# Kernel optimization log

Hardware: AMD Instinct MI355X
Metric: run time of the kernel (lower is better)

The kernel has to match this reference:

```python
import jax, jax.numpy as jnp
import numpy as np

E = 2  # expand_ratio


def _linear_scan(u, a):
    """h_t = a_t * h_{t-1} + u_t along axis 0, h_{-1}=0. Parallel associative scan."""
    def comb(x, y):
        a1, b1 = x
        a2, b2 = y
        return a2 * a1, a2 * b1 + b2
    _, h = jax.lax.associative_scan(comb, (a, u), axis=0)
    return h


def setup_inputs() -> dict:
    key = jax.random.key(0)
    ks = jax.random.split(key, 8)
    n, b, d = 2048, 4, 1024
    s = 1.0 / np.sqrt(d)
    return {
        "x": jax.random.normal(ks[0], (n, b, d), jnp.float32),
        "lower_bound": jax.random.uniform(ks[1], (d,), jnp.float32),
        "W_in": jax.random.normal(ks[2], (d, 3 * d), jnp.float32) * s,
        "b_in": jnp.zeros((3 * d,), jnp.float32),
        "W_out": jax.random.normal(ks[3], (d, d), jnp.float32) * s,
        "b_out": jnp.zeros((d,), jnp.float32),
        "gamma": jnp.ones((d,), jnp.float32),
        "beta": jnp.zeros((d,), jnp.float32),
    }


def reference(x, lower_bound, W_in, b_in, W_out, b_out, gamma, beta):
    n, b, d = x.shape
    h = d // E
    feat = x @ W_in + b_in                      # (n,b,3d)
    inp, og, fg = jnp.split(feat, 3, axis=-1)
    inp = jax.nn.silu(inp)
    og = jax.nn.sigmoid(og)
    fg = jax.nn.sigmoid(fg)
    # reshape (h d) -> h, d=E
    inp = inp.reshape(n, b, h, E)
    og = og.reshape(n, b, h, E)
    fg = fg.reshape(n, b, h, E)
    lb = lower_bound.reshape(h, E)
    lam = lb + (1.0 - lb) * fg                  # (n,b,h,E)
    # outer-product input: (1-lam) outer inp over the E dims -> (n,b,h,E,E)
    u = jnp.einsum('nbhd,nbhe->nbhde', 1.0 - lam, inp)
    a = jnp.broadcast_to(lam[..., None], u.shape)
    u = u.reshape(n, b, h * E * E)
    a = a.reshape(n, b, h * E * E)
    state_fwd = _linear_scan(u, a)
    state_rev = jnp.flip(_linear_scan(jnp.flip(u, 0), jnp.flip(a, 0)), 0)
    state = (state_fwd + state_rev).reshape(n, b, h, E, E)
    out = jnp.einsum('nbhde,nbhd->nbhe', state, og).reshape(n, b, d)
    # layernorm over last dim
    mu = jnp.mean(out, axis=-1, keepdims=True)
    var = jnp.var(out, axis=-1, keepdims=True)
    out = (out - mu) * jax.lax.rsqrt(var + 1e-5) * gamma + beta
    return out @ W_out + b_out
```

## Files before the change

### kernel.cpp

```cpp
#include <hip/hip_runtime.h>

typedef __bf16 bf16x8 __attribute__((ext_vector_type(8)));
typedef float floatx4 __attribute__((ext_vector_type(4)));

#define NCH 128
#define CLEN 16

__device__ __forceinline__ unsigned short f2bf(float f) {
  unsigned int u = __builtin_bit_cast(unsigned int, f);
  u += 0x7fff + ((u >> 16) & 1);
  return (unsigned short)(u >> 16);
}
__device__ __forceinline__ float bf2f(unsigned short u) {
  unsigned int v = (unsigned int)u << 16;
  return __builtin_bit_cast(float, v);
}
__device__ __forceinline__ float bf2f_lo(unsigned int u) {
  return __builtin_bit_cast(float, u << 16);
}
__device__ __forceinline__ float bf2f_hi(unsigned int u) {
  return __builtin_bit_cast(float, u & 0xffff0000u);
}

__device__ __forceinline__ void async_copy16(const void* g, void* l) {
  __builtin_amdgcn_global_load_lds(
      (const __attribute__((address_space(1))) unsigned int*)g,
      (__attribute__((address_space(3))) unsigned int*)l, 16, 0, 0);
}

__global__ void prep_kernel(const float* __restrict__ x, unsigned short* __restrict__ x_bf,
                            const float* __restrict__ Win, unsigned short* __restrict__ winT,
                            const float* __restrict__ Wout, unsigned short* __restrict__ woutT) {
  __shared__ float tile[32][33];
  const int bx = blockIdx.x;
  const int tid = threadIdx.x;
  if (bx < 8192) {
    int i = bx * 256 + tid;
    float4 v = ((const float4*)x)[i];
    ushort4 o;
    o.x = f2bf(v.x); o.y = f2bf(v.y); o.z = f2bf(v.z); o.w = f2bf(v.w);
    ((ushort4*)x_bf)[i] = o;
    return;
  }
  const float* W;
  unsigned short* WT;
  int ncols, n0, k0;
  if (bx < 8192 + 3072) {
    int t2 = bx - 8192;
    W = Win; WT = winT; ncols = 3072;
    n0 = (t2 % 96) * 32; k0 = (t2 / 96) * 32;
  } else {
    int t2 = bx - 8192 - 3072;
    W = Wout; WT = woutT; ncols = 1024;
    n0 = (t2 & 31) * 32; k0 = (t2 >> 5) * 32;
  }
  const int tx = tid & 31, tyb = tid >> 5;
#pragma unroll
  for (int r = 0; r < 4; r++) {
    int ty = tyb + r * 8;
    tile[ty][tx] = W[(size_t)(k0 + ty) * ncols + n0 + tx];
  }
  __syncthreads();
#pragma unroll
  for (int r = 0; r < 4; r++) {
    int ty = tyb + r * 8;
    WT[(size_t)(n0 + ty) * 1024 + k0 + tx] = f2bf(tile[tx][ty]);
  }
}

template <int EPI>
__global__ __launch_bounds__(512, 2) void gemm1_kernel(
    const unsigned short* __restrict__ A, const unsigned short* __restrict__ BT,
    const float* __restrict__ bias, const float* __restrict__ lb,
    float* __restrict__ outf,
    unsigned short* __restrict__ o_inp, unsigned short* __restrict__ o_og,
    unsigned short* __restrict__ o_om) {
  __shared__ alignas(16) char smem[147456];
  const int orig = blockIdx.x;
  const int wg = (EPI == 1) ? (orig & 7) * 96 + (orig >> 3)
                            : (orig & 7) * 32 + (orig >> 3);
  const int m0 = (wg & 63) << 7;
  const int n0 = (wg >> 6) << 8;
  const int tid = threadIdx.x;
  const int lane = tid & 63, wave = tid >> 6;
  const int wm = wave >> 2, wn = wave & 3;
  const int srow = tid >> 3;
  const int sq = (tid & 7) ^ (srow & 7);
  const unsigned short* gA = A + (size_t)(m0 + srow) * 1024 + sq * 8;
  const unsigned short* gB = BT + (size_t)(n0 + srow) * 1024 + sq * 8;
  char* lw = smem + wave * 1024;
  const int aro = (wm * 64 + (lane & 15)) * 128;
  const int bro = (wn * 64 + (lane & 15)) * 128;
  const int qs0 = ((lane >> 4) ^ (lane & 7)) * 16;
  const int qs1 = ((4 + (lane >> 4)) ^ (lane & 7)) * 16;

  floatx4 acc[4][4] = {};
  bf16x8 aF[4][2], bF[4][2];

#define STG(lofs, gh, kk)                                \
  do {                                                   \
    const unsigned short* _g = (gh) + (size_t)(kk) * 64; \
    async_copy16(_g, lw + (lofs));                       \
    async_copy16(_g + 65536, lw + (lofs) + 8192);        \
  } while (0)
#define RA(base, i, s) \
  (*(const bf16x8*)(smem + (base) + aro + (i) * 2048 + ((s) ? qs1 : qs0)))
#define RB(base, j, s) \
  (*(const bf16x8*)(smem + (base) + bro + (j) * 2048 + ((s) ? qs1 : qs0)))
#define BAR __builtin_amdgcn_s_barrier()
#define LGKM0 asm volatile("s_waitcnt lgkmcnt(0)" ::: "memory")
#define VM6 asm volatile("s_waitcnt vmcnt(6)" ::: "memory")
#define MM(d, a, b) d = __builtin_amdgcn_mfma_f32_16x16x32_bf16(a, b, d, 0, 0, 0)

#define TILE(AB, BB, SA, SB, kk)                                               \
  do {                                                                         \
    _Pragma("unroll") for (int i = 0; i < 4; i++) {                            \
      aF[i][0] = RA(AB, i, 0); aF[i][1] = RA(AB, i, 1);                        \
    }                                                                          \
    _Pragma("unroll") for (int j = 0; j < 2; j++) {                            \
      bF[j][0] = RB(BB, j, 0); bF[j][1] = RB(BB, j, 1);                        \
    }                                                                          \
    STG(SA, gA, kk);                                                           \
    STG(SB, gB, kk);                                                           \
    BAR; LGKM0;                                                                \
    __builtin_amdgcn_s_setprio(1);                                             \
    _Pragma("unroll") for (int i = 0; i < 4; i++) {                            \
      _Pragma("unroll") for (int j = 0; j < 2; j++) {                          \
        MM(acc[i][j], aF[i][0], bF[j][0]); MM(acc[i][j], aF[i][1], bF[j][1]);  \
      }                                                                        \
    }                                                                          \
    __builtin_amdgcn_s_setprio(0);                                             \
    BAR;                                                                       \
    _Pragma("unroll") for (int j = 2; j < 4; j++) {                            \
      bF[j][0] = RB(BB, j, 0); bF[j][1] = RB(BB, j, 1);                        \
    }                                                                          \
    STG((SB) + 16384, gB + 131072, kk);                                        \
    BAR; LGKM0;                                                                \
    __builtin_amdgcn_s_setprio(1);                                             \
    _Pragma("unroll") for (int i = 0; i < 4; i++) {                            \
      _Pragma("unroll") for (int j = 2; j < 4; j++) {                          \
        MM(acc[i][j], aF[i][0], bF[j][0]); MM(acc[i][j], aF[i][1], bF[j][1]);  \
      }                                                                        \
    }                                                                          \
    __builtin_amdgcn_s_setprio(0);                                             \
    VM6; BAR;                                                                  \
  } while (0)

  STG(0, gA, 0);
  STG(49152, gB, 0);
  STG(49152 + 16384, gB + 131072, 0);
  STG(16384, gA, 1);
  STG(81920, gB, 1);
  STG(81920 + 16384, gB + 131072, 1);
  VM6;
  BAR;

#pragma unroll 1
  for (int tt = 0; tt < 15; tt += 3) {
    TILE(0, 49152, 32768, 114688, tt + 2);
    TILE(16384, 81920, 0, 49152, tt + 3);
    TILE(32768, 114688, 16384, 81920, (tt + 4 > 15 ? 15 : tt + 4));
  }
  TILE(0, 49152, 32768, 114688, 15);
#undef STG
#undef RA
#undef RB
#undef BAR
#undef LGKM0
#undef VM6
#undef MM
#undef TILE

  asm volatile("s_waitcnt vmcnt(0) lgkmcnt(0)" ::: "memory");
  const int lrw = wm * 16 + (lane >> 4) * 4;
  const int lcw = wn * 64 + (lane & 15);
  const int er = tid >> 4, ec = (tid & 15) * 16;
  const int growb = m0 + (er >> 4) * 64 + (er & 15);
  float bi[4];
#pragma unroll
  for (int j = 0; j < 4; j++) bi[j] = bias[n0 + wn * 64 + j * 16 + (lane & 15)];
  if (EPI == 1) {
    const int seg = n0 >> 10;
    unsigned short* dst = (seg == 0) ? o_inp : (seg == 1) ? o_og : o_om;
    unsigned short* Cs = (unsigned short*)smem;
    float Lv[4];
#pragma unroll
    for (int j = 0; j < 4; j++)
      Lv[j] = (seg == 2) ? lb[(n0 + wn * 64 + j * 16 + (lane & 15)) & 1023] : 0.f;
#pragma unroll
    for (int i = 0; i < 4; i++) {
      __syncthreads();
#pragma unroll
      for (int j = 0; j < 4; j++)
#pragma unroll
        for (int g = 0; g < 4; g++) {
          float v = acc[i][j][g] + bi[j];
          unsigned short ob;
          if (seg == 0) { float s = 1.f / (1.f + __expf(-v)); ob = f2bf(v * s); }
          else if (seg == 1) { float s = 1.f / (1.f + __expf(-v)); ob = f2bf(s); }
          else { float sm = 1.f / (1.f + __expf(v)); ob = f2bf((1.f - Lv[j]) * sm); }
          Cs[(lrw + g) * 264 + lcw + j * 16] = ob;
        }
      __syncthreads();
      uint4 v0 = *(uint4*)&Cs[er * 264 + ec];
      uint4 v1 = *(uint4*)&Cs[er * 264 + ec + 8];
      size_t ro = (size_t)(growb + i * 16) * 1024 + (n0 & 1023) + ec;
      *(uint4*)&dst[ro] = v0;
      *(uint4*)&dst[ro + 8] = v1;
    }
  } else {
    float* Cf = (float*)smem;
#pragma unroll
    for (int i = 0; i < 4; i++) {
      __syncthreads();
#pragma unroll
      for (int j = 0; j < 4; j++)
#pragma unroll
        for (int g = 0; g < 4; g++)
          Cf[(lrw + g) * 264 + lcw + j * 16] = acc[i][j][g] + bi[j];
      __syncthreads();
      size_t ro = (size_t)(growb + i * 16) * 1024 + n0 + ec;
#pragma unroll
      for (int k = 0; k < 4; k++) {
        float4 v = *(float4*)&Cf[er * 264 + ec + k * 4];
        *(float4*)&outf[ro + k * 4] = v;
      }
    }
  }
}

__global__ void scan_passA(const unsigned short* __restrict__ om, const unsigned short* __restrict__ ip,
                           float* __restrict__ sumA, float* __restrict__ sumBf,
                           float* __restrict__ sumBr) {
  int idx = blockIdx.x * 256 + threadIdx.x;
  int h = idx & 511, cb = idx >> 9, b = cb & 3, c = cb >> 2;
  long base = ((long)c * CLEN * 4 + b) * 1024 + 2 * h;
  float p0 = 1.f, p1 = 1.f;
  float s00 = 0.f, s01 = 0.f, s10 = 0.f, s11 = 0.f;
  float r00 = 0.f, r01 = 0.f, r10 = 0.f, r11 = 0.f;
#pragma unroll
  for (int t = 0; t < CLEN; t++) {
    ushort2 l2 = *(const ushort2*)(om + base);
    ushort2 i2 = *(const ushort2*)(ip + base);
    base += 4096;
    float omx = bf2f(l2.x), omy = bf2f(l2.y);
    float ipx = bf2f(i2.x), ipy = bf2f(i2.y);
    float lx = 1.f - omx, ly = 1.f - omy;
    float u00 = omx * ipx, u01 = omx * ipy, u10 = omy * ipx, u11 = omy * ipy;
    r00 += p0 * u00; r01 += p0 * u01; r10 += p1 * u10; r11 += p1 * u11;
    s00 = lx * s00 + u00; s01 = lx * s01 + u01;
    s10 = ly * s10 + u10; s11 = ly * s11 + u11;
    p0 *= lx; p1 *= ly;
  }
  ((float2*)sumA)[idx] = make_float2(p0, p1);
  ((float4*)sumBf)[idx] = make_float4(s00, s01, s10, s11);
  ((float4*)sumBr)[idx] = make_float4(r00, r01, r10, r11);
}

__global__ void scan_b1(const float* __restrict__ sumA, const float* __restrict__ sumBf,
                        const float* __restrict__ sumBr,
                        float* __restrict__ superA, float* __restrict__ superB) {
  int t = blockIdx.x * 256 + threadIdx.x;
  int ch = t & 3, bh = (t >> 2) & 2047, sc = (t >> 13) & 7, dir = t >> 16;
  int dd = ch >> 1;
  float Acc = 1.f, Bcc = 0.f;
  if (dir == 0) {
    for (int i = 0; i < 16; i++) {
      int si = (sc * 16 + i) * 2048 + bh;
      float a = sumA[(size_t)si * 2 + dd];
      float b = sumBf[(size_t)si * 4 + ch];
      Bcc = a * Bcc + b;
      Acc *= a;
    }
  } else {
    for (int i = 15; i >= 0; i--) {
      int si = (sc * 16 + i) * 2048 + bh;
      float a = sumA[(size_t)si * 2 + dd];
      float b = sumBr[(size_t)si * 4 + ch];
      Bcc = a * Bcc + b;
      Acc *= a;
    }
  }
  superA[t] = Acc;
  superB[t] = Bcc;
}

__global__ void scan_b3(const float* __restrict__ sumA, const float* __restrict__ sumBf,
                        const float* __restrict__ sumBr,
                        const float* __restrict__ superA, const float* __restrict__ superB,
                        float* __restrict__ initF, float* __restrict__ initR) {
  int t = blockIdx.x * 256 + threadIdx.x;
  int ch = t & 3, bh = (t >> 2) & 2047, sc = (t >> 13) & 7, dir = t >> 16;
  int dd = ch >> 1;
  float H = 0.f;
  if (dir == 0) {
    for (int s = 0; s < sc; s++) {
      size_t idx = ((size_t)s * 2048 + bh) * 4 + ch;
      H = superA[idx] * H + superB[idx];
    }
    for (int i = 0; i < 16; i++) {
      int si = (sc * 16 + i) * 2048 + bh;
      initF[(size_t)si * 4 + ch] = H;
      H = sumA[(size_t)si * 2 + dd] * H + sumBf[(size_t)si * 4 + ch];
    }
  } else {
    for (int s = 7; s > sc; s--) {
      size_t idx = ((size_t)(8 + s) * 2048 + bh) * 4 + ch;
      H = superA[idx] * H + superB[idx];
    }
    for (int i = 15; i >= 0; i--) {
      int si = (sc * 16 + i) * 2048 + bh;
      initR[(size_t)si * 4 + ch] = H;
      H = sumA[(size_t)si * 2 + dd] * H + sumBr[(size_t)si * 4 + ch];
    }
  }
}

__global__ __launch_bounds__(512) void scanC_ln_kernel(
    const unsigned short* __restrict__ om, const unsigned short* __restrict__ ip,
    const unsigned short* __restrict__ og,
    const float* __restrict__ initF, const float* __restrict__ initR,
    const float* __restrict__ gamma, const float* __restrict__ beta,
    unsigned short* __restrict__ ybf) {
  __shared__ float tile[8][1024];
  __shared__ float ldsG[1024];
  __shared__ float ldsB[1024];
  const int h = threadIdx.x;
  const int cb = blockIdx.x;
  const int b = cb & 3, c = cb >> 2;
  const int idx = cb * 512 + h;
  *(float2*)&ldsG[2 * h] = *(const float2*)(gamma + 2 * h);
  *(float2*)&ldsB[2 * h] = *(const float2*)(beta + 2 * h);
  float4 F = ((const float4*)initF)[idx];
  float4 R = ((const float4*)initR)[idx];
  float outx[CLEN], outy[CLEN];
  unsigned int lS[CLEN], iS[CLEN], oS[CLEN];
  const long base = ((long)c * CLEN * 4 + b) * 1024 + 2 * h;
  float h00 = F.x, h01 = F.y, h10 = F.z, h11 = F.w;
  long p = base;
#pragma unroll
  for (int t = 0; t < CLEN; t++) {
    unsigned int l2 = *(const unsigned int*)(om + p);
    unsigned int i2 = *(const unsigned int*)(ip + p);
    unsigned int o2 = *(const unsigned int*)(og + p);
    p += 4096;
    lS[t] = l2; iS[t] = i2; oS[t] = o2;
    float omx = bf2f_lo(l2), omy = bf2f_hi(l2);
    float ipx = bf2f_lo(i2), ipy = bf2f_hi(i2);
    float ox = bf2f_lo(o2), oy = bf2f_hi(o2);
    float lx = 1.f - omx, ly = 1.f - omy;
    h00 = lx * h00 + omx * ipx; h01 = lx * h01 + omx * ipy;
    h10 = ly * h10 + omy * ipx; h11 = ly * h11 + omy * ipy;
    outx[t] = h00 * ox + h10 * oy;
    outy[t] = h01 * ox + h11 * oy;
  }
  float g00 = R.x, g01 = R.y, g10 = R.z, g11 = R.w;
#pragma unroll
  for (int t = CLEN - 1; t >= 0; t--) {
    unsigned int l2 = lS[t], i2 = iS[t], o2 = oS[t];
    float omx = bf2f_lo(l2), omy = bf2f_hi(l2);
    float ipx = bf2f_lo(i2), ipy = bf2f_hi(i2);
    float ox = bf2f_lo(o2), oy = bf2f_hi(o2);
    float lx = 1.f - omx, ly = 1.f - omy;
    g00 = omx * ipx + lx * g00; g01 = omx * ipy + lx * g01;
    g10 = omy * ipx + ly * g10; g11 = omy * ipy + ly * g11;
    outx[t] += g00 * ox + g10 * oy;
    outy[t] += g01 * ox + g11 * oy;
  }
  const int lane = h & 63, wv = h >> 6;
#pragma unroll
  for (int g = 0; g < CLEN / 8; g++) {
    __syncthreads();
#pragma unroll
    for (int r = 0; r < 8; r++) {
      float2 v2 = make_float2(outx[g * 8 + r], outy[g * 8 + r]);
      *(float2*)&tile[r][2 * h] = v2;
    }
    __syncthreads();
    {
      const int t = g * 8 + wv;
      float4 v[4];
#pragma unroll
      for (int k = 0; k < 4; k++) v[k] = *(const float4*)&tile[wv][lane * 16 + k * 4];
      float s = 0.f, s2 = 0.f;
#pragma unroll
      for (int k = 0; k < 4; k++) {
        s += v[k].x + v[k].y + v[k].z + v[k].w;
        s2 += v[k].x * v[k].x + v[k].y * v[k].y + v[k].z * v[k].z + v[k].w * v[k].w;
      }
#pragma unroll
      for (int off = 1; off < 64; off <<= 1) {
        s += __shfl_xor(s, off);
        s2 += __shfl_xor(s2, off);
      }
      float mean = s * (1.f / 1024.f);
      float var = s2 * (1.f / 1024.f) - mean * mean;
      float rstd = rsqrtf(var + 1e-5f);
      unsigned short o16[16];
#pragma unroll
      for (int k = 0; k < 4; k++) {
        float* vv = (float*)&v[k];
#pragma unroll
        for (int e = 0; e < 4; e++) {
          int ch = lane * 16 + k * 4 + e;
          o16[k * 4 + e] = f2bf((vv[e] - mean) * rstd * ldsG[ch] + ldsB[ch]);
        }
      }
      size_t rowo = ((size_t)(c * CLEN + t) * 4 + b) * 1024 + lane * 16;
      *(uint4*)(ybf + rowo) = *(uint4*)&o16[0];
      *(uint4*)(ybf + rowo + 8) = *(uint4*)&o16[8];
    }
  }
}

extern "C" void kernel_launch(void* const* d_in, const int* in_sizes, int n_in,
                              void* d_out, int out_size, void* d_ws, size_t ws_size,
                              hipStream_t stream) {
  const float* x = (const float*)d_in[0];
  const float* lb = (const float*)d_in[1];
  const float* Win = (const float*)d_in[2];
  const float* bin = (const float*)d_in[3];
  const float* Wout = (const float*)d_in[4];
  const float* bout = (const float*)d_in[5];
  const float* gamma = (const float*)d_in[6];
  const float* beta = (const float*)d_in[7];
  float* out = (float*)d_out;

  char* ws = (char*)d_ws;
  size_t off = 0;
  auto alloc = [&](size_t bytes) {
    void* p = ws + off;
    off += (bytes + 255) & ~(size_t)255;
    return p;
  };
  unsigned short* x_bf = (unsigned short*)alloc(8192ull * 1024 * 2);
  unsigned short* winT = (unsigned short*)alloc(3072ull * 1024 * 2);
  unsigned short* woutT = (unsigned short*)alloc(1024ull * 1024 * 2);
  unsigned short* inp_b = (unsigned short*)alloc(8192ull * 1024 * 2);
  unsigned short* og_b = (unsigned short*)alloc(8192ull * 1024 * 2);
  unsigned short* om_b = (unsigned short*)alloc(8192ull * 1024 * 2);
  unsigned short* y_bf = (unsigned short*)alloc(8192ull * 1024 * 2);
  float* sumA = (float*)alloc((size_t)NCH * 4 * 512 * 2 * 4);
  float* sumBf = (float*)alloc((size_t)NCH * 4 * 512 * 4 * 4);
  float* sumBr = (float*)alloc((size_t)NCH * 4 * 512 * 4 * 4);
  float* initF = (float*)alloc((size_t)NCH * 4 * 512 * 4 * 4);
  float* initR = (float*)alloc((size_t)NCH * 4 * 512 * 4 * 4);
  float* superA = (float*)alloc(131072ull * 4);
  float* superB = (float*)alloc(131072ull * 4);

  prep_kernel<<<12288, 256, 0, stream>>>(x, x_bf, Win, winT, Wout, woutT);
  gemm1_kernel<1><<<768, 512, 0, stream>>>(x_bf, winT, bin, lb, nullptr, inp_b, og_b, om_b);
  scan_passA<<<(NCH * 4 * 512) / 256, 256, 0, stream>>>(om_b, inp_b, sumA, sumBf, sumBr);
  scan_b1<<<512, 256, 0, stream>>>(sumA, sumBf, sumBr, superA, superB);
  scan_b3<<<512, 256, 0, stream>>>(sumA, sumBf, sumBr, superA, superB, initF, initR);
  scanC_ln_kernel<<<NCH * 4, 512, 0, stream>>>(om_b, inp_b, og_b, initF, initR, gamma, beta, y_bf);
  gemm1_kernel<0><<<256, 512, 0, stream>>>(y_bf, woutT, bout, nullptr, out, nullptr, nullptr, nullptr);
}
```

Baseline: 239.7 us.

## Fuse three scan stages into one persistent kernel with grid barriers

Merges scan_passA, scan_b1 and scan_b3 into a single kernel of 512 blocks by 512 threads that separates the stages with atomic-counter grid barriers instead of kernel launches. The goal is to remove two kernel launch gaps and the tail drain between these small kernels. It relies on all 512 blocks being co-resident, which should hold on a 256-CU part, adds a memset of the counter, and leaves half of each block idle in the later stages.

```diff
diff --git a/kernel.cpp b/kernel.cpp
--- a/kernel.cpp
+++ b/kernel.cpp
@@ -26,6 +26,19 @@
   __builtin_amdgcn_global_load_lds(
       (const __attribute__((address_space(1))) unsigned int*)g,
       (__attribute__((address_space(3))) unsigned int*)l, 16, 0, 0);
+}
+
+__device__ __forceinline__ void grid_bar(unsigned* cnt, unsigned target) {
+  __syncthreads();
+  __threadfence();
+  if (threadIdx.x == 0) {
+    __hip_atomic_fetch_add(cnt, 1u, __ATOMIC_ACQ_REL, __HIP_MEMORY_SCOPE_AGENT);
+    while (__hip_atomic_load(cnt, __ATOMIC_ACQUIRE, __HIP_MEMORY_SCOPE_AGENT) < target) {
+      __builtin_amdgcn_s_sleep(4);
+    }
+  }
+  __syncthreads();
+  __threadfence();
 }
 
 __global__ void prep_kernel(const float* __restrict__ x, unsigned short* __restrict__ x_bf,
@@ -229,89 +242,89 @@
   }
 }
 
-__global__ void scan_passA(const unsigned short* __restrict__ om, const unsigned short* __restrict__ ip,
-                           float* __restrict__ sumA, float* __restrict__ sumBf,
-                           float* __restrict__ sumBr) {
-  int idx = blockIdx.x * 256 + threadIdx.x;
-  int h = idx & 511, cb = idx >> 9, b = cb & 3, c = cb >> 2;
-  long base = ((long)c * CLEN * 4 + b) * 1024 + 2 * h;
-  float p0 = 1.f, p1 = 1.f;
-  float s00 = 0.f, s01 = 0.f, s10 = 0.f, s11 = 0.f;
-  float r00 = 0.f, r01 = 0.f, r10 = 0.f, r11 = 0.f;
-#pragma unroll
-  for (int t = 0; t < CLEN; t++) {
-    ushort2 l2 = *(const ushort2*)(om + base);
-    ushort2 i2 = *(const ushort2*)(ip + base);
-    base += 4096;
-    float omx = bf2f(l2.x), omy = bf2f(l2.y);
-    float ipx = bf2f(i2.x), ipy = bf2f(i2.y);
-    float lx = 1.f - omx, ly = 1.f - omy;
-    float u00 = omx * ipx, u01 = omx * ipy, u10 = omy * ipx, u11 = omy * ipy;
-    r00 += p0 * u00; r01 += p0 * u01; r10 += p1 * u10; r11 += p1 * u11;
-    s00 = lx * s00 + u00; s01 = lx * s01 + u01;
-    s10 = ly * s10 + u10; s11 = ly * s11 + u11;
-    p0 *= lx; p1 *= ly;
-  }
-  ((float2*)sumA)[idx] = make_float2(p0, p1);
-  ((float4*)sumBf)[idx] = make_float4(s00, s01, s10, s11);
-  ((float4*)sumBr)[idx] = make_float4(r00, r01, r10, r11);
-}
-
-__global__ void scan_b1(const float* __restrict__ sumA, const float* __restrict__ sumBf,
-                        const float* __restrict__ sumBr,
-                        float* __restrict__ superA, float* __restrict__ superB) {
-  int t = blockIdx.x * 256 + threadIdx.x;
-  int ch = t & 3, bh = (t >> 2) & 2047, sc = (t >> 13) & 7, dir = t >> 16;
-  int dd = ch >> 1;
-  float Acc = 1.f, Bcc = 0.f;
-  if (dir == 0) {
-    for (int i = 0; i < 16; i++) {
-      int si = (sc * 16 + i) * 2048 + bh;
-      float a = sumA[(size_t)si * 2 + dd];
-      float b = sumBf[(size_t)si * 4 + ch];
-      Bcc = a * Bcc + b;
-      Acc *= a;
-    }
-  } else {
-    for (int i = 15; i >= 0; i--) {
-      int si = (sc * 16 + i) * 2048 + bh;
-      float a = sumA[(size_t)si * 2 + dd];
-      float b = sumBr[(size_t)si * 4 + ch];
-      Bcc = a * Bcc + b;
-      Acc *= a;
-    }
-  }
-  superA[t] = Acc;
-  superB[t] = Bcc;
-}
-
-__global__ void scan_b3(const float* __restrict__ sumA, const float* __restrict__ sumBf,
-                        const float* __restrict__ sumBr,
-                        const float* __restrict__ superA, const float* __restrict__ superB,
-                        float* __restrict__ initF, float* __restrict__ initR) {
-  int t = blockIdx.x * 256 + threadIdx.x;
-  int ch = t & 3, bh = (t >> 2) & 2047, sc = (t >> 13) & 7, dir = t >> 16;
-  int dd = ch >> 1;
-  float H = 0.f;
-  if (dir == 0) {
-    for (int s = 0; s < sc; s++) {
-      size_t idx = ((size_t)s * 2048 + bh) * 4 + ch;
-      H = superA[idx] * H + superB[idx];
-    }
-    for (int i = 0; i < 16; i++) {
-      int si = (sc * 16 + i) * 2048 + bh;
-      initF[(size_t)si * 4 + ch] = H;
-      H = sumA[(size_t)si * 2 + dd] * H + sumBf[(size_t)si * 4 + ch];
-    }
-  } else {
-    for (int s = 7; s > sc; s--) {
-      size_t idx = ((size_t)(8 + s) * 2048 + bh) * 4 + ch;
-      H = superA[idx] * H + superB[idx];
-    }
-    for (int i = 15; i >= 0; i--) {
-      int si = (sc * 16 + i) * 2048 + bh;
-      initR[(size_t)si * 4 + ch] = H;
-      H = sumA[(size_t)si * 2 + dd] * H + sumBr[(size_t)si * 4 + ch];
+__global__ __launch_bounds__(512) void scan_mid_kernel(
+    const unsigned short* __restrict__ om, const unsigned short* __restrict__ ip,
+    float* __restrict__ sumA, float* __restrict__ sumBf, float* __restrict__ sumBr,
+    float* __restrict__ superA, float* __restrict__ superB,
+    float* __restrict__ initF, float* __restrict__ initR,
+    unsigned* __restrict__ barcnt) {
+  {
+    int idx = blockIdx.x * 512 + threadIdx.x;
+    int h = idx & 511, cb = idx >> 9;
+    long base = ((long)(cb >> 2) * CLEN * 4 + (cb & 3)) * 1024 + 2 * h;
+    float p0 = 1.f, p1 = 1.f;
+    float s00 = 0.f, s01 = 0.f, s10 = 0.f, s11 = 0.f;
+    float r00 = 0.f, r01 = 0.f, r10 = 0.f, r11 = 0.f;
+#pragma unroll
+    for (int t = 0; t < CLEN; t++) {
+      ushort2 l2 = *(const ushort2*)(om + base);
+      ushort2 i2 = *(const ushort2*)(ip + base);
+      base += 4096;
+      float omx = bf2f(l2.x), omy = bf2f(l2.y);
+      float ipx = bf2f(i2.x), ipy = bf2f(i2.y);
+      float lx = 1.f - omx, ly = 1.f - omy;
+      float u00 = omx * ipx, u01 = omx * ipy, u10 = omy * ipx, u11 = omy * ipy;
+      r00 += p0 * u00; r01 += p0 * u01; r10 += p1 * u10; r11 += p1 * u11;
+      s00 = lx * s00 + u00; s01 = lx * s01 + u01;
+      s10 = ly * s10 + u10; s11 = ly * s11 + u11;
+      p0 *= lx; p1 *= ly;
+    }
+    ((float2*)sumA)[idx] = make_float2(p0, p1);
+    ((float4*)sumBf)[idx] = make_float4(s00, s01, s10, s11);
+    ((float4*)sumBr)[idx] = make_float4(r00, r01, r10, r11);
+  }
+  grid_bar(barcnt, gridDim.x);
+  if (threadIdx.x < 256) {
+    int t = blockIdx.x * 256 + threadIdx.x;
+    int ch = t & 3, bh = (t >> 2) & 2047, sc = (t >> 13) & 7, dir = t >> 16;
+    int dd = ch >> 1;
+    float Acc = 1.f, Bcc = 0.f;
+    if (dir == 0) {
+      for (int i = 0; i < 16; i++) {
+        int si = (sc * 16 + i) * 2048 + bh;
+        float a = sumA[(size_t)si * 2 + dd];
+        float b = sumBf[(size_t)si * 4 + ch];
+        Bcc = a * Bcc + b;
+        Acc *= a;
+      }
+    } else {
+      for (int i = 15; i >= 0; i--) {
+        int si = (sc * 16 + i) * 2048 + bh;
+        float a = sumA[(size_t)si * 2 + dd];
+        float b = sumBr[(size_t)si * 4 + ch];
+        Bcc = a * Bcc + b;
+        Acc *= a;
+      }
+    }
+    superA[t] = Acc;
+    superB[t] = Bcc;
+  }
+  grid_bar(barcnt, 2 * gridDim.x);
+  if (threadIdx.x < 256) {
+    int t = blockIdx.x * 256 + threadIdx.x;
+    int ch = t & 3, bh = (t >> 2) & 2047, sc = (t >> 13) & 7, dir = t >> 16;
+    int dd = ch >> 1;
+    float H = 0.f;
+    if (dir == 0) {
+      for (int s = 0; s < sc; s++) {
+        size_t idx = ((size_t)s * 2048 + bh) * 4 + ch;
+        H = superA[idx] * H + superB[idx];
+      }
+      for (int i = 0; i < 16; i++) {
+        int si = (sc * 16 + i) * 2048 + bh;
+        initF[(size_t)si * 4 + ch] = H;
+        H = sumA[(size_t)si * 2 + dd] * H + sumBf[(size_t)si * 4 + ch];
+      }
+    } else {
+      for (int s = 7; s > sc; s--) {
+        size_t idx = ((size_t)(8 + s) * 2048 + bh) * 4 + ch;
+        H = superA[idx] * H + superB[idx];
+      }
+      for (int i = 15; i >= 0; i--) {
+        int si = (sc * 16 + i) * 2048 + bh;
+        initR[(size_t)si * 4 + ch] = H;
+        H = sumA[(size_t)si * 2 + dd] * H + sumBr[(size_t)si * 4 + ch];
+      }
     }
   }
 }
@@ -447,12 +460,13 @@
   float* initR = (float*)alloc((size_t)NCH * 4 * 512 * 4 * 4);
   float* superA = (float*)alloc(131072ull * 4);
   float* superB = (float*)alloc(131072ull * 4);
-
+  unsigned* barcnt = (unsigned*)alloc(256);
+
+  hipMemsetAsync(barcnt, 0, sizeof(unsigned), stream);
   prep_kernel<<<12288, 256, 0, stream>>>(x, x_bf, Win, winT, Wout, woutT);
   gemm1_kernel<1><<<768, 512, 0, stream>>>(x_bf, winT, bin, lb, nullptr, inp_b, og_b, om_b);
-  scan_passA<<<(NCH * 4 * 512) / 256, 256, 0, stream>>>(om_b, inp_b, sumA, sumBf, sumBr);
-  scan_b1<<<512, 256, 0, stream>>>(sumA, sumBf, sumBr, superA, superB);
-  scan_b3<<<512, 256, 0, stream>>>(sumA, sumBf, sumBr, superA, superB, initF, initR);
+  scan_mid_kernel<<<512, 512, 0, stream>>>(om_b, inp_b, sumA, sumBf, sumBr, superA, superB,
+                                           initF, initR, barcnt);
   scanC_ln_kernel<<<NCH * 4, 512, 0, stream>>>(om_b, inp_b, og_b, initF, initR, gamma, beta, y_bf);
   gemm1_kernel<0><<<256, 512, 0, stream>>>(y_bf, woutT, bout, nullptr, out, nullptr, nullptr, nullptr);
 }
```

Result: slower. 543.9 us (+127.0%).
